# Performance work log

Hardware: AMD Instinct MI355X
Metric: run time of the kernel (lower is better)

## Reference

```python
import jax, jax.numpy as jnp
import numpy as np

B, H, S, D = 4, 16, 2048, 128

def setup_inputs() -> dict:
    key = jax.random.key(0)
    kq, kk, kv, ks = jax.random.split(key, 4)
    return {
        "query": jax.random.normal(kq, (B, H, S, D), dtype=jnp.float32),
        "key": jax.random.normal(kk, (B, H, S, D), dtype=jnp.float32),
        "value": jax.random.normal(kv, (B, H, S, D), dtype=jnp.float32),
        "scale_factor": jax.random.normal(ks, (B, H, 1, 1), dtype=jnp.float32),
    }

def reference(query, key, value, scale_factor):
    # qk = Q @ K^T : [B,H,S,S]
    qk = jnp.einsum("bhsd,bhtd->bhst", query, key)
    scaled_qk = qk * scale_factor  # per-head broadcast scale
    softmax_qk = jax.nn.softmax(scaled_qk, axis=-1)
    # dropout treated as identity (eval-mode determinism for baseline)
    out = jnp.einsum("bhst,bhtd->bhsd", softmax_qk, value)
    return out
```

## Files before the change

### kernel.cpp

```cpp
#include <hip/hip_runtime.h>
#include <hip/hip_bf16.h>


typedef __bf16 bf16;
typedef __attribute__((ext_vector_type(4))) __bf16 bf16x4;
typedef __attribute__((ext_vector_type(8))) __bf16 bf16x8;
typedef __attribute__((ext_vector_type(4))) float f32x4;

constexpr int S_  = 2048;
constexpr int D_  = 128;
constexpr int BM  = 64;
constexpr int BN  = 32;
constexpr int NIT = S_ / BN;
constexpr int PK  = D_ + 8;
constexpr int PVT = 32;
constexpr int PP  = BN + 8;

constexpr size_t WS_KL   = 16777216;
constexpr size_t WS_VT   = 33554432;
constexpr size_t WS_NEED = 100663296;

template <int CTRL>
__device__ __forceinline__ float dpp_fmax_step(float x) {
    int yi = __builtin_amdgcn_update_dpp(
        __float_as_int(x), __float_as_int(x), CTRL, 0xf, 0xf, false);
    return fmaxf(x, __int_as_float(yi));
}
template <int CTRL>
__device__ __forceinline__ float dpp_fadd_step(float x) {
    int yi = __builtin_amdgcn_update_dpp(
        __float_as_int(x), __float_as_int(x), CTRL, 0xf, 0xf, false);
    return x + __int_as_float(yi);
}
__device__ __forceinline__ float row16_max(float x) {
    x = dpp_fmax_step<0xB1>(x);
    x = dpp_fmax_step<0x4E>(x);
    x = dpp_fmax_step<0x141>(x);
    x = dpp_fmax_step<0x140>(x);
    return x;
}
__device__ __forceinline__ float row16_sum(float x) {
    x = dpp_fadd_step<0xB1>(x);
    x = dpp_fadd_step<0x4E>(x);
    x = dpp_fadd_step<0x141>(x);
    x = dpp_fadd_step<0x140>(x);
    return x;
}

__global__ __launch_bounds__(256) void prepack(
    const float* __restrict__ kg, const float* __restrict__ vg,
    bf16* __restrict__ ws)
{
    const int gid = blockIdx.x * 256 + threadIdx.x;
    if (gid < 2097152) {
        const int u  = gid & 15;
        const int rg = gid >> 4;
        const float* src = kg + (size_t)rg * D_ + (u << 3);
        float x[8];
        *(float4*)&x[0] = *(const float4*)src;
        *(float4*)&x[4] = *(const float4*)(src + 4);
        bf16x8 h8, l8;
#pragma unroll
        for (int j = 0; j < 8; ++j) {
            bf16 h = (bf16)x[j];
            h8[j] = h;
            l8[j] = (bf16)(x[j] - (float)h);
        }
        const size_t di = (size_t)rg * 128 + (u << 3);
        *(bf16x8*)&ws[di]         = h8;
        *(bf16x8*)&ws[WS_KL + di] = l8;
    } else {
        const int g2 = gid - 2097152;
        const int i  = g2 & 511;
        const int tg = g2 >> 9;
        const int p  = i & 15;
        const int c  = i >> 4;
        const float* src = vg + ((size_t)tg * BN + 2 * p) * D_ + c * 4;
        float4 a0 = *(const float4*)src;
        float4 a1 = *(const float4*)(src + D_);
        const float* x0 = (const float*)&a0;
        const float* x1 = (const float*)&a1;
        bf16* vt = ws + WS_VT + (size_t)tg * 4096;
#pragma unroll
        for (int j = 0; j < 4; ++j) {
            union { ushort2 u2; bf16 b[2]; } pr;
            pr.b[0] = (bf16)x0[j];
            pr.b[1] = (bf16)x1[j];
            *(ushort2*)&vt[(c * 4 + j) * BN + 2 * p] = pr.u2;
        }
    }
}

__global__ __launch_bounds__(256, 4) void attn_fwd(
    const float* __restrict__ q, const bf16* __restrict__ ws,
    const float* __restrict__ sc, float* __restrict__ out)
{
    __shared__ __align__(16) bf16 Kh[BN * PK];
    __shared__ __align__(16) bf16 Kl[BN * PK];
    __shared__ __align__(16) bf16 Vs[D_ * PVT];
    __shared__ __align__(16) bf16 Ps[4 * 16 * PP];

    const int tid  = threadIdx.x;
    const int wave = tid >> 6;
    const int lane = tid & 63;
    const int l16  = lane & 15;
    const int quad = lane >> 4;

    const int bid = blockIdx.x;
    const int idx = bid >> 3;
    const int bh  = ((bid & 7) << 3) | (idx >> 5);
    const int qt  = idx & 31;

    const float scale = sc[bh] * 1.44269504088896f;

    const float* qbase = q + ((size_t)bh * S_ + (size_t)qt * BM) * D_;
    const bf16* khp = ws +         (size_t)bh * 262144 + tid * 8;
    const bf16* klp = ws + WS_KL + (size_t)bh * 262144 + tid * 8;
    const bf16* vtp = ws + WS_VT + (size_t)bh * 262144 + tid * 8;

    bf16x8 qh[4], ql[4];
    {
        const float* qrow = qbase + (size_t)(wave * 16 + l16) * D_ + quad * 8;
#pragma unroll
        for (int ks = 0; ks < 4; ++ks) {
            float x[8];
            *(float4*)&x[0] = *(const float4*)(qrow + ks * 32);
            *(float4*)&x[4] = *(const float4*)(qrow + ks * 32 + 4);
#pragma unroll
            for (int j = 0; j < 8; ++j) {
                float xs = x[j] * scale;
                bf16 h = (bf16)xs;
                qh[ks][j] = h;
                ql[ks][j] = (bf16)(xs - (float)h);
            }
        }
    }

    f32x4 O[8];
#pragma unroll
    for (int i = 0; i < 8; ++i) O[i] = (f32x4){0.f, 0.f, 0.f, 0.f};
    float mrow[4] = {-1e30f, -1e30f, -1e30f, -1e30f};
    float Lp[4]   = {0.f, 0.f, 0.f, 0.f};

    bf16x8 rKh[2], rKl[2], rVt[2];

#define LOADT(t)                                                          \
    {                                                                     \
        const size_t toff = (size_t)(t) * 4096;                           \
        rKh[0] = *(const bf16x8*)(khp + toff);                            \
        rKh[1] = *(const bf16x8*)(khp + toff + 2048);                     \
        rKl[0] = *(const bf16x8*)(klp + toff);                            \
        rKl[1] = *(const bf16x8*)(klp + toff + 2048);                     \
        rVt[0] = *(const bf16x8*)(vtp + toff);                            \
        rVt[1] = *(const bf16x8*)(vtp + toff + 2048);                     \
    }

#define WRITET()                                                          \
    {                                                                     \
        _Pragma("unroll")                                                 \
        for (int j = 0; j < 2; ++j) {                                     \
            int i = tid + j * 256;                                        \
            *(bf16x8*)&Kh[(i >> 4) * PK + (i & 15) * 8] = rKh[j];         \
            *(bf16x8*)&Kl[(i >> 4) * PK + (i & 15) * 8] = rKl[j];         \
            *(bf16x8*)&Vs[i * 8] = rVt[j];                                \
        }                                                                 \
    }

    LOADT(0);
    WRITET();
    LOADT(1);
    __syncthreads();

    for (int it = 0; it < NIT; ++it) {
        f32x4 sacc[2];
        sacc[0] = (f32x4){0.f, 0.f, 0.f, 0.f};
        sacc[1] = (f32x4){0.f, 0.f, 0.f, 0.f};
        __builtin_amdgcn_s_setprio(1);
#pragma unroll
        for (int ks = 0; ks < 4; ++ks) {
#pragma unroll
            for (int nb = 0; nb < 2; ++nb) {
                int off = (nb * 16 + l16) * PK + ks * 32 + quad * 8;
                bf16x8 kh = *(const bf16x8*)&Kh[off];
                bf16x8 kl = *(const bf16x8*)&Kl[off];
                sacc[nb] = __builtin_amdgcn_mfma_f32_16x16x32_bf16(qh[ks], kh, sacc[nb], 0, 0, 0);
                sacc[nb] = __builtin_amdgcn_mfma_f32_16x16x32_bf16(qh[ks], kl, sacc[nb], 0, 0, 0);
                sacc[nb] = __builtin_amdgcn_mfma_f32_16x16x32_bf16(ql[ks], kh, sacc[nb], 0, 0, 0);
            }
        }
        __builtin_amdgcn_s_setprio(0);

        float m0r[4];
        bool grow = false;
#pragma unroll
        for (int r = 0; r < 4; ++r) {
            float m0 = row16_max(fmaxf(sacc[0][r], sacc[1][r]));
            m0r[r] = m0;
            grow |= (m0 - mrow[r] > 8.0f);
        }
        if (__any(grow)) {
#pragma unroll
            for (int r = 0; r < 4; ++r) {
                float mnew  = fmaxf(mrow[r], m0r[r]);
                float alpha = __builtin_amdgcn_exp2f(mrow[r] - mnew);
                mrow[r] = mnew;
                Lp[r] *= alpha;
#pragma unroll
                for (int d = 0; d < 8; ++d) O[d][r] *= alpha;
            }
        }
        float p0[4], p1[4];
#pragma unroll
        for (int r = 0; r < 4; ++r) {
            float e0 = __builtin_amdgcn_exp2f(sacc[0][r] - mrow[r]);
            float e1 = __builtin_amdgcn_exp2f(sacc[1][r] - mrow[r]);
            p0[r] = e0; p1[r] = e1;
            Lp[r] += e0 + e1;
        }

        bf16* pw = &Ps[wave * 16 * PP];
#pragma unroll
        for (int r = 0; r < 4; ++r) {
            pw[(quad * 4 + r) * PP + l16]      = (bf16)p0[r];
            pw[(quad * 4 + r) * PP + 16 + l16] = (bf16)p1[r];
        }

        {
            bf16x8 pa = *(const bf16x8*)&pw[l16 * PP + quad * 8];
            __builtin_amdgcn_s_setprio(1);
#pragma unroll
            for (int d = 0; d < 8; ++d) {
                bf16x8 vb = *(const bf16x8*)&Vs[(d * 16 + l16) * PVT + quad * 8];
                O[d] = __builtin_amdgcn_mfma_f32_16x16x32_bf16(pa, vb, O[d], 0, 0, 0);
            }
            __builtin_amdgcn_s_setprio(0);
        }

        if (it == NIT - 1) break;
        __syncthreads();
        WRITET();
        if (it + 2 < NIT) LOADT(it + 2);
        __syncthreads();
    }

    float rl[4];
#pragma unroll
    for (int r = 0; r < 4; ++r)
        rl[r] = 1.0f / row16_sum(Lp[r]);
    float* og = out + ((size_t)bh * S_ + (size_t)qt * BM + wave * 16) * D_;
#pragma unroll
    for (int d = 0; d < 8; ++d)
#pragma unroll
        for (int r = 0; r < 4; ++r)
            og[(quad * 4 + r) * D_ + d * 16 + l16] = O[d][r] * rl[r];
}

__global__ __launch_bounds__(256, 4) void attn_fwd_fb(
    const float* __restrict__ q, const float* __restrict__ kg,
    const float* __restrict__ vg, const float* __restrict__ sc,
    float* __restrict__ out)
{
    constexpr int FPVT = BN + 8;

    __shared__ __align__(16) bf16 Kh[BN * PK];
    __shared__ __align__(16) bf16 Kl[BN * PK];
    __shared__ __align__(16) bf16 Vs[D_ * FPVT];
    __shared__ __align__(16) bf16 Ps2[4 * 16 * PP];

    const int tid  = threadIdx.x;
    const int wave = tid >> 6;
    const int lane = tid & 63;
    const int l16  = lane & 15;
    const int quad = lane >> 4;

    const int qt = blockIdx.x;
    const int bh = blockIdx.y;

    const float scale = sc[bh] * 1.44269504088896f;

    const float* qbase = q  + ((size_t)bh * S_ + (size_t)qt * BM) * D_;
    const float* kbase = kg + (size_t)bh * S_ * D_;
    const float* vbase = vg + (size_t)bh * S_ * D_;

    bf16x8 qh[4], ql[4];
    {
        const float* qrow = qbase + (size_t)(wave * 16 + l16) * D_ + quad * 8;
#pragma unroll
        for (int ks = 0; ks < 4; ++ks) {
            float x[8];
            *(float4*)&x[0] = *(const float4*)(qrow + ks * 32);
            *(float4*)&x[4] = *(const float4*)(qrow + ks * 32 + 4);
#pragma unroll
            for (int j = 0; j < 8; ++j) {
                float xs = x[j] * scale;
                bf16 h = (bf16)xs;
                qh[ks][j] = h;
                ql[ks][j] = (bf16)(xs - (float)h);
            }
        }
    }

    f32x4 O[8];
#pragma unroll
    for (int i = 0; i < 8; ++i) O[i] = (f32x4){0.f, 0.f, 0.f, 0.f};
    float mrow[4] = {-1e30f, -1e30f, -1e30f, -1e30f};
    float Lp[4]   = {0.f, 0.f, 0.f, 0.f};

    for (int it = 0; it < NIT; ++it) {
        __syncthreads();
        {
            const float* kt = kbase + (size_t)it * BN * D_;
#pragma unroll
            for (int r = 0; r < 4; ++r) {
                int i = tid + r * 256;
                int row = i >> 5, c = i & 31;
                float4 v = *(const float4*)(kt + row * D_ + c * 4);
                const float* x = (const float*)&v;
                bf16x4 h4, l4;
#pragma unroll
                for (int j = 0; j < 4; ++j) {
                    bf16 h = (bf16)x[j];
                    h4[j] = h;
                    l4[j] = (bf16)(x[j] - (float)h);
                }
                *(bf16x4*)&Kh[row * PK + c * 4] = h4;
                *(bf16x4*)&Kl[row * PK + c * 4] = l4;
            }
            const float* vt = vbase + (size_t)it * BN * D_;
#pragma unroll
            for (int r = 0; r < 2; ++r) {
                int i = tid + r * 256;
                int p = i & 15;
                int c = i >> 4;
                const float* v0 = vt + (2 * p) * D_ + c * 4;
                float4 a0 = *(const float4*)v0;
                float4 a1 = *(const float4*)(v0 + D_);
                const float* x0 = (const float*)&a0;
                const float* x1 = (const float*)&a1;
#pragma unroll
                for (int j = 0; j < 4; ++j) {
                    union { ushort2 u; bf16 b[2]; } pr;
                    pr.b[0] = (bf16)x0[j];
                    pr.b[1] = (bf16)x1[j];
                    *(ushort2*)&Vs[(c * 4 + j) * FPVT + 2 * p] = pr.u;
                }
            }
        }
        __syncthreads();

        f32x4 sacc[2];
        sacc[0] = (f32x4){0.f, 0.f, 0.f, 0.f};
        sacc[1] = (f32x4){0.f, 0.f, 0.f, 0.f};
#pragma unroll
        for (int ks = 0; ks < 4; ++ks) {
#pragma unroll
            for (int nb = 0; nb < 2; ++nb) {
                int off = (nb * 16 + l16) * PK + ks * 32 + quad * 8;
                bf16x8 kh = *(const bf16x8*)&Kh[off];
                bf16x8 kl = *(const bf16x8*)&Kl[off];
                sacc[nb] = __builtin_amdgcn_mfma_f32_16x16x32_bf16(qh[ks], kh, sacc[nb], 0, 0, 0);
                sacc[nb] = __builtin_amdgcn_mfma_f32_16x16x32_bf16(qh[ks], kl, sacc[nb], 0, 0, 0);
                sacc[nb] = __builtin_amdgcn_mfma_f32_16x16x32_bf16(ql[ks], kh, sacc[nb], 0, 0, 0);
            }
        }

        float p0[4], p1[4];
#pragma unroll
        for (int r = 0; r < 4; ++r) {
            float m0 = fmaxf(sacc[0][r], sacc[1][r]);
#pragma unroll
            for (int off = 8; off >= 1; off >>= 1)
                m0 = fmaxf(m0, __shfl_xor(m0, off, 64));
            float mnew  = fmaxf(mrow[r], m0);
            float alpha = __builtin_amdgcn_exp2f(mrow[r] - mnew);
            mrow[r] = mnew;
            float e0 = __builtin_amdgcn_exp2f(sacc[0][r] - mnew);
            float e1 = __builtin_amdgcn_exp2f(sacc[1][r] - mnew);
            p0[r] = e0; p1[r] = e1;
            Lp[r] = Lp[r] * alpha + (e0 + e1);
#pragma unroll
            for (int d = 0; d < 8; ++d) O[d][r] *= alpha;
        }

        bf16* pw = &Ps2[wave * 16 * PP];
#pragma unroll
        for (int r = 0; r < 4; ++r) {
            pw[(quad * 4 + r) * PP + l16]      = (bf16)p0[r];
            pw[(quad * 4 + r) * PP + 16 + l16] = (bf16)p1[r];
        }
        {
            bf16x8 pa = *(const bf16x8*)&pw[l16 * PP + quad * 8];
#pragma unroll
            for (int d = 0; d < 8; ++d) {
                bf16x8 vb = *(const bf16x8*)&Vs[(d * 16 + l16) * FPVT + quad * 8];
                O[d] = __builtin_amdgcn_mfma_f32_16x16x32_bf16(pa, vb, O[d], 0, 0, 0);
            }
        }
    }

    float rl[4];
#pragma unroll
    for (int r = 0; r < 4; ++r) {
        float L = Lp[r];
#pragma unroll
        for (int off = 8; off >= 1; off >>= 1)
            L += __shfl_xor(L, off, 64);
        rl[r] = 1.0f / L;
    }
    float* og = out + ((size_t)bh * S_ + (size_t)qt * BM + wave * 16) * D_;
#pragma unroll
    for (int d = 0; d < 8; ++d)
#pragma unroll
        for (int r = 0; r < 4; ++r)
            og[(quad * 4 + r) * D_ + d * 16 + l16] = O[d][r] * rl[r];
}

extern "C" void kernel_launch(void* const* d_in, const int* in_sizes, int n_in,
                              void* d_out, int out_size, void* d_ws, size_t ws_size,
                              hipStream_t stream) {
    const float* q  = (const float*)d_in[0];
    const float* k  = (const float*)d_in[1];
    const float* v  = (const float*)d_in[2];
    const float* sc = (const float*)d_in[3];
    float* o = (float*)d_out;
    if (d_ws && ws_size >= WS_NEED) {
        bf16* ws = (bf16*)d_ws;
        prepack<<<16384, 256, 0, stream>>>(k, v, ws);
        attn_fwd<<<2048, 256, 0, stream>>>(q, ws, sc, o);
    } else {
        attn_fwd_fb<<<dim3(S_ / BM, 64), 256, 0, stream>>>(q, k, v, sc, o);
    }
}
```

Measured before the change: 524.8 us.

## Double query rows per wave to reuse K/V tiles across two M-blocks

Raises the query tile from 64 to 128 rows so each wave handles two 16-row blocks. Every K and V fragment read from shared memory then feeds two MFMAs, which halves the grid and the K/V traffic per query row. The V shared tile gets a padded row stride to reduce bank conflicts. In exchange, register pressure roughly doubles for the accumulators and Q fragments, occupancy drops to 2 blocks per SIMD-group, and fewer blocks means coarser load balance.

```diff
diff --git a/kernel.cpp b/kernel.cpp
--- a/kernel.cpp
+++ b/kernel.cpp
@@ -9,11 +9,11 @@
 
 constexpr int S_  = 2048;
 constexpr int D_  = 128;
-constexpr int BM  = 64;
+constexpr int BM  = 128;
 constexpr int BN  = 32;
 constexpr int NIT = S_ / BN;
 constexpr int PK  = D_ + 8;
-constexpr int PVT = 32;
+constexpr int PVT = BN + 8;
 constexpr int PP  = BN + 8;
 
 constexpr size_t WS_KL   = 16777216;
@@ -91,14 +91,14 @@
     }
 }
 
-__global__ __launch_bounds__(256, 4) void attn_fwd(
+__global__ __launch_bounds__(256, 2) void attn_fwd(
     const float* __restrict__ q, const bf16* __restrict__ ws,
     const float* __restrict__ sc, float* __restrict__ out)
 {
     __shared__ __align__(16) bf16 Kh[BN * PK];
     __shared__ __align__(16) bf16 Kl[BN * PK];
     __shared__ __align__(16) bf16 Vs[D_ * PVT];
-    __shared__ __align__(16) bf16 Ps[4 * 16 * PP];
+    __shared__ __align__(16) bf16 Ps[4 * 32 * PP];
 
     const int tid  = threadIdx.x;
     const int wave = tid >> 6;
@@ -108,8 +108,8 @@
 
     const int bid = blockIdx.x;
     const int idx = bid >> 3;
-    const int bh  = ((bid & 7) << 3) | (idx >> 5);
-    const int qt  = idx & 31;
+    const int bh  = ((bid & 7) << 3) | (idx >> 4);
+    const int qt  = idx & 15;
 
     const float scale = sc[bh] * 1.44269504088896f;
 
@@ -118,9 +118,11 @@
     const bf16* klp = ws + WS_KL + (size_t)bh * 262144 + tid * 8;
     const bf16* vtp = ws + WS_VT + (size_t)bh * 262144 + tid * 8;
 
-    bf16x8 qh[4], ql[4];
-    {
-        const float* qrow = qbase + (size_t)(wave * 16 + l16) * D_ + quad * 8;
+    bf16x8 qh[2][4], ql[2][4];
+#pragma unroll
+    for (int mb = 0; mb < 2; ++mb) {
+        const float* qrow =
+            qbase + (size_t)(wave * 32 + mb * 16 + l16) * D_ + quad * 8;
 #pragma unroll
         for (int ks = 0; ks < 4; ++ks) {
             float x[8];
@@ -130,17 +132,22 @@
             for (int j = 0; j < 8; ++j) {
                 float xs = x[j] * scale;
                 bf16 h = (bf16)xs;
-                qh[ks][j] = h;
-                ql[ks][j] = (bf16)(xs - (float)h);
-            }
-        }
-    }
-
-    f32x4 O[8];
-#pragma unroll
-    for (int i = 0; i < 8; ++i) O[i] = (f32x4){0.f, 0.f, 0.f, 0.f};
-    float mrow[4] = {-1e30f, -1e30f, -1e30f, -1e30f};
-    float Lp[4]   = {0.f, 0.f, 0.f, 0.f};
+                qh[mb][ks][j] = h;
+                ql[mb][ks][j] = (bf16)(xs - (float)h);
+            }
+        }
+    }
+
+    f32x4 O[2][8];
+#pragma unroll
+    for (int mb = 0; mb < 2; ++mb)
+#pragma unroll
+        for (int i = 0; i < 8; ++i) O[mb][i] = (f32x4){0.f, 0.f, 0.f, 0.f};
+    float mrow[2][4], Lp[2][4];
+#pragma unroll
+    for (int mb = 0; mb < 2; ++mb)
+#pragma unroll
+        for (int r = 0; r < 4; ++r) { mrow[mb][r] = -1e30f; Lp[mb][r] = 0.f; }
 
     bf16x8 rKh[2], rKl[2], rVt[2];
 
@@ -162,7 +169,7 @@
             int i = tid + j * 256;                                        \
             *(bf16x8*)&Kh[(i >> 4) * PK + (i & 15) * 8] = rKh[j];         \
             *(bf16x8*)&Kl[(i >> 4) * PK + (i & 15) * 8] = rKl[j];         \
-            *(bf16x8*)&Vs[i * 8] = rVt[j];                                \
+            *(bf16x8*)&Vs[(i >> 2) * PVT + (i & 3) * 8] = rVt[j];         \
         }                                                                 \
     }
 
@@ -172,9 +179,12 @@
     __syncthreads();
 
     for (int it = 0; it < NIT; ++it) {
-        f32x4 sacc[2];
-        sacc[0] = (f32x4){0.f, 0.f, 0.f, 0.f};
-        sacc[1] = (f32x4){0.f, 0.f, 0.f, 0.f};
+        f32x4 sacc[2][2];
+#pragma unroll
+        for (int mb = 0; mb < 2; ++mb)
+#pragma unroll
+            for (int nb = 0; nb < 2; ++nb)
+                sacc[mb][nb] = (f32x4){0.f, 0.f, 0.f, 0.f};
         __builtin_amdgcn_s_setprio(1);
 #pragma unroll
         for (int ks = 0; ks < 4; ++ks) {
@@ -183,55 +193,68 @@
                 int off = (nb * 16 + l16) * PK + ks * 32 + quad * 8;
                 bf16x8 kh = *(const bf16x8*)&Kh[off];
                 bf16x8 kl = *(const bf16x8*)&Kl[off];
-                sacc[nb] = __builtin_amdgcn_mfma_f32_16x16x32_bf16(qh[ks], kh, sacc[nb], 0, 0, 0);
-                sacc[nb] = __builtin_amdgcn_mfma_f32_16x16x32_bf16(qh[ks], kl, sacc[nb], 0, 0, 0);
-                sacc[nb] = __builtin_amdgcn_mfma_f32_16x16x32_bf16(ql[ks], kh, sacc[nb], 0, 0, 0);
+                sacc[0][nb] = __builtin_amdgcn_mfma_f32_16x16x32_bf16(qh[0][ks], kh, sacc[0][nb], 0, 0, 0);
+                sacc[0][nb] = __builtin_amdgcn_mfma_f32_16x16x32_bf16(qh[0][ks], kl, sacc[0][nb], 0, 0, 0);
+                sacc[0][nb] = __builtin_amdgcn_mfma_f32_16x16x32_bf16(ql[0][ks], kh, sacc[0][nb], 0, 0, 0);
+                sacc[1][nb] = __builtin_amdgcn_mfma_f32_16x16x32_bf16(qh[1][ks], kh, sacc[1][nb], 0, 0, 0);
+                sacc[1][nb] = __builtin_amdgcn_mfma_f32_16x16x32_bf16(qh[1][ks], kl, sacc[1][nb], 0, 0, 0);
+                sacc[1][nb] = __builtin_amdgcn_mfma_f32_16x16x32_bf16(ql[1][ks], kh, sacc[1][nb], 0, 0, 0);
             }
         }
         __builtin_amdgcn_s_setprio(0);
 
-        float m0r[4];
+        float m0r[2][4];
         bool grow = false;
 #pragma unroll
-        for (int r = 0; r < 4; ++r) {
-            float m0 = row16_max(fmaxf(sacc[0][r], sacc[1][r]));
-            m0r[r] = m0;
-            grow |= (m0 - mrow[r] > 8.0f);
-        }
+        for (int mb = 0; mb < 2; ++mb)
+#pragma unroll
+            for (int r = 0; r < 4; ++r) {
+                float m0 = row16_max(fmaxf(sacc[mb][0][r], sacc[mb][1][r]));
+                m0r[mb][r] = m0;
+                grow |= (m0 - mrow[mb][r] > 8.0f);
+            }
         if (__any(grow)) {
 #pragma unroll
+            for (int mb = 0; mb < 2; ++mb)
+#pragma unroll
+                for (int r = 0; r < 4; ++r) {
+                    float mnew  = fmaxf(mrow[mb][r], m0r[mb][r]);
+                    float alpha = __builtin_amdgcn_exp2f(mrow[mb][r] - mnew);
+                    mrow[mb][r] = mnew;
+                    Lp[mb][r] *= alpha;
+#pragma unroll
+                    for (int d = 0; d < 8; ++d) O[mb][d][r] *= alpha;
+                }
+        }
+        float p0[2][4], p1[2][4];
+#pragma unroll
+        for (int mb = 0; mb < 2; ++mb)
+#pragma unroll
             for (int r = 0; r < 4; ++r) {
-                float mnew  = fmaxf(mrow[r], m0r[r]);
-                float alpha = __builtin_amdgcn_exp2f(mrow[r] - mnew);
-                mrow[r] = mnew;
-                Lp[r] *= alpha;
-#pragma unroll
-                for (int d = 0; d < 8; ++d) O[d][r] *= alpha;
-            }
-        }
-        float p0[4], p1[4];
-#pragma unroll
-        for (int r = 0; r < 4; ++r) {
-            float e0 = __builtin_amdgcn_exp2f(sacc[0][r] - mrow[r]);
-            float e1 = __builtin_amdgcn_exp2f(sacc[1][r] - mrow[r]);
-            p0[r] = e0; p1[r] = e1;
-            Lp[r] += e0 + e1;
-        }
-
-        bf16* pw = &Ps[wave * 16 * PP];
-#pragma unroll
-        for (int r = 0; r < 4; ++r) {
-            pw[(quad * 4 + r) * PP + l16]      = (bf16)p0[r];
-            pw[(quad * 4 + r) * PP + 16 + l16] = (bf16)p1[r];
-        }
+                float e0 = __builtin_amdgcn_exp2f(sacc[mb][0][r] - mrow[mb][r]);
+                float e1 = __builtin_amdgcn_exp2f(sacc[mb][1][r] - mrow[mb][r]);
+                p0[mb][r] = e0; p1[mb][r] = e1;
+                Lp[mb][r] += e0 + e1;
+            }
+
+        bf16* pw = &Ps[wave * 32 * PP];
+#pragma unroll
+        for (int mb = 0; mb < 2; ++mb)
+#pragma unroll
+            for (int r = 0; r < 4; ++r) {
+                pw[(mb * 16 + quad * 4 + r) * PP + l16]      = (bf16)p0[mb][r];
+                pw[(mb * 16 + quad * 4 + r) * PP + 16 + l16] = (bf16)p1[mb][r];
+            }
 
         {
-            bf16x8 pa = *(const bf16x8*)&pw[l16 * PP + quad * 8];
+            bf16x8 pa0 = *(const bf16x8*)&pw[l16 * PP + quad * 8];
+            bf16x8 pa1 = *(const bf16x8*)&pw[(16 + l16) * PP + quad * 8];
             __builtin_amdgcn_s_setprio(1);
 #pragma unroll
             for (int d = 0; d < 8; ++d) {
                 bf16x8 vb = *(const bf16x8*)&Vs[(d * 16 + l16) * PVT + quad * 8];
-                O[d] = __builtin_amdgcn_mfma_f32_16x16x32_bf16(pa, vb, O[d], 0, 0, 0);
+                O[0][d] = __builtin_amdgcn_mfma_f32_16x16x32_bf16(pa0, vb, O[0][d], 0, 0, 0);
+                O[1][d] = __builtin_amdgcn_mfma_f32_16x16x32_bf16(pa1, vb, O[1][d], 0, 0, 0);
             }
             __builtin_amdgcn_s_setprio(0);
         }
@@ -243,16 +266,21 @@
         __syncthreads();
     }
 
-    float rl[4];
-#pragma unroll
-    for (int r = 0; r < 4; ++r)
-        rl[r] = 1.0f / row16_sum(Lp[r]);
-    float* og = out + ((size_t)bh * S_ + (size_t)qt * BM + wave * 16) * D_;
-#pragma unroll
-    for (int d = 0; d < 8; ++d)
+    float rl[2][4];
+#pragma unroll
+    for (int mb = 0; mb < 2; ++mb)
 #pragma unroll
         for (int r = 0; r < 4; ++r)
-            og[(quad * 4 + r) * D_ + d * 16 + l16] = O[d][r] * rl[r];
+            rl[mb][r] = 1.0f / row16_sum(Lp[mb][r]);
+    float* og = out + ((size_t)bh * S_ + (size_t)qt * BM + wave * 32) * D_;
+#pragma unroll
+    for (int mb = 0; mb < 2; ++mb)
+#pragma unroll
+        for (int d = 0; d < 8; ++d)
+#pragma unroll
+            for (int r = 0; r < 4; ++r)
+                og[(mb * 16 + quad * 4 + r) * D_ + d * 16 + l16] =
+                    O[mb][d][r] * rl[mb][r];
 }
 
 __global__ __launch_bounds__(256, 4) void attn_fwd_fb(
@@ -260,11 +288,11 @@
     const float* __restrict__ vg, const float* __restrict__ sc,
     float* __restrict__ out)
 {
-    constexpr int FPVT = BN + 8;
+    constexpr int FBM = 64;
 
     __shared__ __align__(16) bf16 Kh[BN * PK];
     __shared__ __align__(16) bf16 Kl[BN * PK];
-    __shared__ __align__(16) bf16 Vs[D_ * FPVT];
+    __shared__ __align__(16) bf16 Vs[D_ * PVT];
     __shared__ __align__(16) bf16 Ps2[4 * 16 * PP];
 
     const int tid  = threadIdx.x;
@@ -278,7 +306,7 @@
 
     const float scale = sc[bh] * 1.44269504088896f;
 
-    const float* qbase = q  + ((size_t)bh * S_ + (size_t)qt * BM) * D_;
+    const float* qbase = q  + ((size_t)bh * S_ + (size_t)qt * FBM) * D_;
     const float* kbase = kg + (size_t)bh * S_ * D_;
     const float* vbase = vg + (size_t)bh * S_ * D_;
 
@@ -342,7 +370,7 @@
                     union { ushort2 u; bf16 b[2]; } pr;
                     pr.b[0] = (bf16)x0[j];
                     pr.b[1] = (bf16)x1[j];
-                    *(ushort2*)&Vs[(c * 4 + j) * FPVT + 2 * p] = pr.u;
+                    *(ushort2*)&Vs[(c * 4 + j) * PVT + 2 * p] = pr.u;
                 }
             }
         }
@@ -392,7 +420,7 @@
             bf16x8 pa = *(const bf16x8*)&pw[l16 * PP + quad * 8];
 #pragma unroll
             for (int d = 0; d < 8; ++d) {
-                bf16x8 vb = *(const bf16x8*)&Vs[(d * 16 + l16) * FPVT + quad * 8];
+                bf16x8 vb = *(const bf16x8*)&Vs[(d * 16 + l16) * PVT + quad * 8];
                 O[d] = __builtin_amdgcn_mfma_f32_16x16x32_bf16(pa, vb, O[d], 0, 0, 0);
             }
         }
@@ -407,7 +435,7 @@
             L += __shfl_xor(L, off, 64);
         rl[r] = 1.0f / L;
     }
-    float* og = out + ((size_t)bh * S_ + (size_t)qt * BM + wave * 16) * D_;
+    float* og = out + ((size_t)bh * S_ + (size_t)qt * FBM + wave * 16) * D_;
 #pragma unroll
     for (int d = 0; d < 8; ++d)
 #pragma unroll
@@ -426,8 +454,8 @@
     if (d_ws && ws_size >= WS_NEED) {
         bf16* ws = (bf16*)d_ws;
         prepack<<<16384, 256, 0, stream>>>(k, v, ws);
-        attn_fwd<<<2048, 256, 0, stream>>>(q, ws, sc, o);
+        attn_fwd<<<1024, 256, 0, stream>>>(q, ws, sc, o);
     } else {
-        attn_fwd_fb<<<dim3(S_ / BM, 64), 256, 0, stream>>>(q, k, v, sc, o);
-    }
-}
+        attn_fwd_fb<<<dim3(S_ / 64, 64), 256, 0, stream>>>(q, k, v, sc, o);
+    }
+}
```

Result: no change. 524.0 us (-0.2%).
